# Kernel optimization log

Hardware: AMD Instinct MI355X
Metric: run time of the kernel (lower is better)

The kernel has to match this reference:

```python
import jax, jax.numpy as jnp
import numpy as np

EMB_DIM = 256
N_PTS = 2048  # decoder output points
LN_EPS = 1e-5


def setup_inputs() -> dict:
    key = jax.random.key(0)
    ks = jax.random.split(key, 20)
    B, N = 16, 4096

    def w(k, shape, fan_in):
        return (jax.random.normal(k, shape, dtype=jnp.float32) / np.sqrt(fan_in)).astype(jnp.float32)

    return {
        "in_pc": jax.random.normal(ks[0], (B, N, 3), dtype=jnp.float32),
        # encoder: 1x1 convs == per-point linear over channels
        "conv1_w": w(ks[1], (64, 3), 3),     "conv1_b": jnp.zeros((64,), jnp.float32),
        "conv2_w": w(ks[2], (128, 64), 64),  "conv2_b": jnp.zeros((128,), jnp.float32),
        "conv3_w": w(ks[3], (1024, 256), 256), "conv3_b": jnp.zeros((1024,), jnp.float32),
        "fc_enc_w": w(ks[4], (EMB_DIM, 1024), 1024), "fc_enc_b": jnp.zeros((EMB_DIM,), jnp.float32),
        # decoder
        "fc1_w": w(ks[5], (512, EMB_DIM), EMB_DIM), "fc1_b": jnp.zeros((512,), jnp.float32),
        "fc2_w": w(ks[6], (1024, 512), 512),        "fc2_b": jnp.zeros((1024,), jnp.float32),
        "fc3_w": w(ks[7], (3 * N_PTS, 1024), 1024), "fc3_b": jnp.zeros((3 * N_PTS,), jnp.float32),
        "ln_g": jnp.ones((3 * N_PTS,), jnp.float32), "ln_b": jnp.zeros((3 * N_PTS,), jnp.float32),
    }


def _pointwise(x, w, b):
    # x: (B, Cin, N), w: (Cout, Cin) -> (B, Cout, N)   (Conv1d with kernel=1)
    return jnp.einsum('bcn,oc->bon', x, w) + b[None, :, None]


def _chamfer(p, q):
    # p: (B,N,3), q: (B,M,3). Squared-L2 pairwise distance + min reductions.
    p2 = jnp.sum(p * p, axis=-1)                      # (B,N)
    q2 = jnp.sum(q * q, axis=-1)                      # (B,M)
    d = p2[:, :, None] + q2[:, None, :] - 2.0 * jnp.einsum('bnd,bmd->bnm', p, q)  # (B,N,M)
    return jnp.min(d, axis=2), jnp.min(d, axis=1)     # (B,N), (B,M)


def reference(in_pc, conv1_w, conv1_b, conv2_w, conv2_b, conv3_w, conv3_b,
              fc_enc_w, fc_enc_b, fc1_w, fc1_b, fc2_w, fc2_b, fc3_w, fc3_b,
              ln_g, ln_b):
    B, N, _ = in_pc.shape
    # ---- encoder ----
    xyz = jnp.transpose(in_pc, (0, 2, 1))            # (B,3,N)
    x = jax.nn.relu(_pointwise(xyz, conv1_w, conv1_b))   # (B,64,N)
    x = jax.nn.relu(_pointwise(x, conv2_w, conv2_b))     # (B,128,N)
    gfeat = jnp.max(x, axis=2, keepdims=True)            # (B,128,1) adaptive_max_pool1d(x,1)
    x0 = jnp.concatenate([x, jnp.broadcast_to(gfeat, (B, 128, N))], axis=1)  # (B,256,N)
    x = jax.nn.relu(_pointwise(x0, conv3_w, conv3_b))    # (B,1024,N)
    x = jnp.max(x, axis=2)                               # (B,1024)
    emb = x @ fc_enc_w.T + fc_enc_b                      # (B,EMB_DIM)
    # ---- decoder ----
    h = jax.nn.relu(emb @ fc1_w.T + fc1_b)               # (B,512)
    h = jax.nn.relu(h @ fc2_w.T + fc2_b)                 # (B,1024)
    h = h @ fc3_w.T + fc3_b                              # (B,3*N_PTS)
    mu = jnp.mean(h, axis=-1, keepdims=True)
    var = jnp.mean((h - mu) ** 2, axis=-1, keepdims=True)
    h = (h - mu) * jax.lax.rsqrt(var + LN_EPS) * ln_g + ln_b
    out_pc = h.reshape(B, -1, 3)                         # (B,N_PTS,3)
    # ---- chamfer reconstruction loss ----
    d1, d2 = _chamfer(in_pc, out_pc)
    loss = jnp.mean(d1) + jnp.mean(d2)
    return (x0, emb, out_pc, loss)
```

## Files before the change

### kernel.cpp

```cpp
#include <hip/hip_runtime.h>

#define OUT_X0   0
#define OUT_EMB  16777216
#define OUT_OPC  16781312
#define OUT_LOSS 16879616

#define OFF_GFEAT 0
#define OFF_POOL  8192
#define OFF_GCON  73728
#define OFF_EMB   139264
#define OFF_HD1   155648
#define OFF_HD2   188416
#define OFF_H3    253952
#define OFF_OPC   647168
#define OFF_D1M   1040384
#define OFF_D2M   1302528
#define OFF_PS    1433600
#define OFF_W3BF  1433984
#define OFF_CNT   1958272
#define H2_BYTES  (16u*1024*1024)

typedef short short8 __attribute__((ext_vector_type(8)));
typedef float f32x4  __attribute__((ext_vector_type(4)));

__device__ __forceinline__ unsigned short f2bf(float f){
  unsigned u = __float_as_uint(f);
  return (unsigned short)((u + 0x7FFFu + ((u >> 16) & 1u)) >> 16);
}

__global__ __launch_bounds__(256) void conv12_mfma(
    const float* __restrict__ in_pc,
    const float* __restrict__ w1, const float* __restrict__ b1,
    const float* __restrict__ w2, const float* __restrict__ b2,
    float* __restrict__ x0, unsigned short* __restrict__ h2b,
    unsigned* __restrict__ gfeatU,
    const float* __restrict__ w3, unsigned* __restrict__ w3bf)
{
  __shared__ unsigned short w2s[8192];
  __shared__ unsigned short h1s[8192];
  __shared__ float b2s[128];
  __shared__ unsigned gmax[128];
  int tid = threadIdx.x, bid = blockIdx.x;
  if (bid >= 512){
    int i = (bid-512)*256 + tid;
    float2 v = ((const float2*)w3)[i];
    w3bf[i] = (unsigned)f2bf(v.x) | ((unsigned)f2bf(v.y)<<16);
    return;
  }
  int b = bid >> 5;
  int nt0 = (bid & 31)*128;
  for (int i = tid; i < 2048; i += 256){
    int ch = i >> 4, q = i & 15;
    float4 v = ((const float4*)w2)[i];
    unsigned lo = (unsigned)f2bf(v.x) | ((unsigned)f2bf(v.y)<<16);
    unsigned hi = (unsigned)f2bf(v.z) | ((unsigned)f2bf(v.w)<<16);
    int byte = (ch*128 + q*8) ^ ((ch&7)<<4);
    *(uint2*)((char*)w2s + byte) = make_uint2(lo, hi);
  }
  if (tid < 128){ b2s[tid] = b2[tid]; gmax[tid] = 0u; }
  {
    int pt = tid & 127;
    int qb = (tid >> 7) * 16;
    int idx = b*4096 + nt0 + pt;
    const float* p = in_pc + (size_t)idx*3;
    float px=p[0], py=p[1], pz=p[2];
    unsigned hp[16];
    #pragma unroll
    for (int q=0;q<16;q++){
      int c = (qb + q)*2;
      float v0 = fmaxf(fmaf(w1[c*3  ],px, fmaf(w1[c*3+1],py, fmaf(w1[c*3+2],pz, b1[c  ]))), 0.f);
      float v1 = fmaxf(fmaf(w1[c*3+3],px, fmaf(w1[c*3+4],py, fmaf(w1[c*3+5],pz, b1[c+1]))), 0.f);
      hp[q] = (unsigned)f2bf(v0) | ((unsigned)f2bf(v1)<<16);
    }
    #pragma unroll
    for (int t=0;t<4;t++){
      int byte = (pt*128 + qb*4 + t*16) ^ ((pt&7)<<4);
      *(uint4*)((char*)h1s + byte) = make_uint4(hp[t*4],hp[t*4+1],hp[t*4+2],hp[t*4+3]);
    }
  }
  __syncthreads();
  int lane = tid & 63, w = tid >> 6;
  int g = lane >> 4, p15 = lane & 15;
  f32x4 acc[8][2] = {};
  #pragma unroll
  for (int ks=0; ks<2; ks++){
    int kb = (ks*32 + g*8)*2;
    short8 bfr[2];
    #pragma unroll
    for (int nf=0;nf<2;nf++){
      int pt = w*32 + nf*16 + p15;
      bfr[nf] = *(const short8*)((const char*)h1s + ((pt*128 + kb) ^ ((pt&7)<<4)));
    }
    #pragma unroll
    for (int mf=0;mf<8;mf++){
      int ch = mf*16 + p15;
      short8 af = *(const short8*)((const char*)w2s + ((ch*128 + kb) ^ ((ch&7)<<4)));
      acc[mf][0] = __builtin_amdgcn_mfma_f32_16x16x32_bf16(af, bfr[0], acc[mf][0], 0,0,0);
      acc[mf][1] = __builtin_amdgcn_mfma_f32_16x16x32_bf16(af, bfr[1], acc[mf][1], 0,0,0);
    }
  }
  int n_base = nt0 + w*32;
  #pragma unroll
  for (int mf=0; mf<8; mf++){
    int ch0 = mf*16 + g*4;
    float bias[4];
    #pragma unroll
    for (int j=0;j<4;j++) bias[j] = b2s[ch0+j];
    float vm[4] = {0.f,0.f,0.f,0.f};
    #pragma unroll
    for (int nf=0; nf<2; nf++){
      int n = n_base + nf*16 + p15;
      float v[4];
      #pragma unroll
      for (int j=0;j<4;j++){
        v[j] = fmaxf(acc[mf][nf][j] + bias[j], 0.f);
        vm[j] = fmaxf(vm[j], v[j]);
        x0[((size_t)(b*256 + ch0 + j))*4096 + n] = v[j];
      }
      unsigned lo = (unsigned)f2bf(v[0]) | ((unsigned)f2bf(v[1])<<16);
      unsigned hi = (unsigned)f2bf(v[2]) | ((unsigned)f2bf(v[3])<<16);
      *(uint2*)&h2b[((size_t)(b*4096 + n))*128 + ch0] = make_uint2(lo, hi);
    }
    #pragma unroll
    for (int j=0;j<4;j++){
      float m = vm[j];
      m = fmaxf(m, __shfl_xor(m,1));
      m = fmaxf(m, __shfl_xor(m,2));
      m = fmaxf(m, __shfl_xor(m,4));
      m = fmaxf(m, __shfl_xor(m,8));
      if (p15==0) atomicMax(&gmax[ch0+j], __float_as_uint(m));
    }
  }
  __syncthreads();
  if (tid < 128) atomicMax(&gfeatU[b*128 + tid], gmax[tid]);
}

__global__ __launch_bounds__(256) void bcast_gcon(
    const unsigned* __restrict__ gfeatU, float* __restrict__ x0,
    const float* __restrict__ w3, const float* __restrict__ b3,
    float* __restrict__ gcon)
{
  __shared__ float gf[2048];
  int tid = threadIdx.x;
  if (blockIdx.x < 8192){
    unsigned U = blockIdx.x*256 + tid;
    int n4 = U & 1023, c = (U >> 10) & 127, b = U >> 17;
    float g = __uint_as_float(gfeatU[b*128+c]);
    float4 v = {g,g,g,g};
    ((float4*)x0)[(((size_t)b*256 + 128 + c)*4096)/4 + n4] = v;
  } else {
    for (int i=tid;i<2048;i+=256) gf[i] = __uint_as_float(gfeatU[i]);
    __syncthreads();
    int o = (blockIdx.x - 8192)*256 + tid;
    float bias = b3[o];
    float acc[16];
    #pragma unroll
    for (int b=0;b<16;b++) acc[b]=bias;
    for (int c=0;c<128;c++){
      float wv = w3[(size_t)o*256 + 128 + c];
      #pragma unroll
      for (int b=0;b<16;b++) acc[b] += gf[b*128+c]*wv;
    }
    #pragma unroll
    for (int b=0;b<16;b++) gcon[b*1024+o] = acc[b];
  }
}

__global__ __launch_bounds__(512) void conv3_pool(
    const unsigned short* __restrict__ h2b, const unsigned short* __restrict__ w3b,
    const float* __restrict__ gcon, unsigned* __restrict__ pooled)
{
  __shared__ unsigned short Al[128*128];
  __shared__ unsigned short Bl[128*128];
  int mt = blockIdx.x, b = blockIdx.y;
  int tid = threadIdx.x;
  {
    const uint4* src = (const uint4*)(h2b + ((size_t)b*4096 + mt*128)*128);
    #pragma unroll
    for (int i=0;i<4;i++){
      int idx = i*512 + tid;
      int r = idx>>4, kc = idx&15;
      uint4 v = src[idx];
      int byte = (r*256 + kc*16) ^ ((r&7)<<4);
      *(uint4*)((char*)Al + byte) = v;
    }
  }
  int lane = tid & 63, wid = tid >> 6;
  int wm = wid >> 2, wn = wid & 3;
  int mbase = wm*64, nbase = wn*32;
  for (int nt=0; nt<8; nt++){
    if (nt) __syncthreads();
    {
      #pragma unroll
      for (int i=0;i<4;i++){
        int idx = i*512 + tid;
        int c = idx>>4, kc = idx&15;
        uint4 v = *(const uint4*)(w3b + ((size_t)(nt*128+c)*256 + kc*8));
        int byte = (c*256 + kc*16) ^ ((c&7)<<4);
        *(uint4*)((char*)Bl + byte) = v;
      }
    }
    __syncthreads();
    f32x4 acc[4][2] = {};
    #pragma unroll
    for (int ks=0;ks<4;ks++){
      int kb = (ks*32 + (lane>>4)*8)*2;
      short8 af[4], bfr[2];
      #pragma unroll
      for (int mi=0;mi<4;mi++){
        int row = mbase + mi*16 + (lane&15);
        af[mi] = *(const short8*)((const char*)Al + ((row*256 + kb) ^ ((row&7)<<4)));
      }
      #pragma unroll
      for (int ni=0;ni<2;ni++){
        int col = nbase + ni*16 + (lane&15);
        bfr[ni] = *(const short8*)((const char*)Bl + ((col*256 + kb) ^ ((col&7)<<4)));
      }
      #pragma unroll
      for (int mi=0;mi<4;mi++){
        #pragma unroll
        for (int ni=0;ni<2;ni++)
          acc[mi][ni] = __builtin_amdgcn_mfma_f32_16x16x32_bf16(af[mi], bfr[ni], acc[mi][ni], 0,0,0);
      }
    }
    #pragma unroll
    for (int ni=0;ni<2;ni++){
      int o = nt*128 + nbase + ni*16 + (lane&15);
      float g = gcon[b*1024 + o];
      float m = 0.f;
      #pragma unroll
      for (int mi=0;mi<4;mi++){
        f32x4 a = acc[mi][ni];
        #pragma unroll
        for (int r=0;r<4;r++){ float v = a[r]+g; m = fmaxf(m, v); }
      }
      m = fmaxf(m, 0.f);
      m = fmaxf(m, __shfl_xor(m, 16));
      m = fmaxf(m, __shfl_xor(m, 32));
      if (lane < 16) atomicMax(&pooled[(size_t)b*1024+o], __float_as_uint(m));
    }
  }
}

__global__ __launch_bounds__(256) void conv12_f32(
    const float* __restrict__ in_pc,
    const float* __restrict__ w1, const float* __restrict__ b1,
    const float* __restrict__ w2, const float* __restrict__ b2,
    float* __restrict__ x0, unsigned* __restrict__ gfeatU)
{
  __shared__ unsigned gmax[32];
  int tid = threadIdx.x;
  if (tid < 32) gmax[tid] = 0u;
  __syncthreads();
  int idx = blockIdx.x*256 + tid;
  int b = idx >> 12, n = idx & 4095;
  int gy = blockIdx.y;
  int lane = tid & 63;
  const float* p = in_pc + (size_t)idx*3;
  float px=p[0], py=p[1], pz=p[2];
  float h1[64];
  #pragma unroll
  for (int c=0;c<64;c++)
    h1[c] = fmaxf(w1[c*3]*px + w1[c*3+1]*py + w1[c*3+2]*pz + b1[c], 0.f);
  #pragma unroll
  for (int j=0;j<32;j++){
    int o = gy*32 + j;
    float a = b2[o];
    #pragma unroll
    for (int c=0;c<64;c++) a += w2[o*64+c]*h1[c];
    a = fmaxf(a, 0.f);
    x0[((size_t)b*256 + o)*4096 + n] = a;
    float m = a;
    #pragma unroll
    for (int off=32; off; off>>=1) m = fmaxf(m, __shfl_xor(m, off));
    if (lane==0) atomicMax(&gmax[j], __float_as_uint(m));
  }
  __syncthreads();
  if (tid < 32) atomicMax(&gfeatU[b*128 + gy*32 + tid], gmax[tid]);
}

__global__ __launch_bounds__(256) void conv3n(
    const float* __restrict__ x0, const unsigned* __restrict__ gfeatU,
    const float* __restrict__ w3, const float* __restrict__ b3,
    unsigned* __restrict__ pooled)
{
  __shared__ float wrow[8][256];
  int b = blockIdx.x >> 7, og = (blockIdx.x & 127)*8, tid = threadIdx.x;
  for (int i=tid;i<2048;i+=256){ int j=i>>8, c=i&255; wrow[j][c]=w3[(size_t)(og+j)*256+c]; }
  __syncthreads();
  float gconst[8];
  #pragma unroll
  for (int j=0;j<8;j++){
    float g = b3[og+j];
    for (int c=0;c<128;c++) g += __uint_as_float(gfeatU[b*128+c])*wrow[j][128+c];
    gconst[j] = g;
  }
  const float* xb = x0 + (size_t)b*256*4096;
  float m[8];
  #pragma unroll
  for (int j=0;j<8;j++) m[j]=0.f;
  for (int n=tid;n<4096;n+=256){
    float v[8];
    #pragma unroll
    for (int j=0;j<8;j++) v[j]=gconst[j];
    for (int c=0;c<128;c++){
      float xv = xb[(size_t)c*4096 + n];
      #pragma unroll
      for (int j=0;j<8;j++) v[j] += xv*wrow[j][c];
    }
    #pragma unroll
    for (int j=0;j<8;j++) m[j] = fmaxf(m[j], v[j]);
  }
  #pragma unroll
  for (int j=0;j<8;j++){
    float v = m[j];
    for (int off=32; off; off>>=1) v = fmaxf(v, __shfl_xor(v, off));
    if ((tid&63)==0) atomicMax(&pooled[(size_t)b*1024+og+j], __float_as_uint(v));
  }
}

template<bool RELU>
__global__ __launch_bounds__(256) void fc_wave16(
    const float* __restrict__ A, const float* __restrict__ W,
    const float* __restrict__ bias, float* __restrict__ out,
    float* __restrict__ out2, int K, int O)
{
  int lane = threadIdx.x & 63, w = threadIdx.x >> 6;
  int o = blockIdx.x*4 + w;
  const float* Wr = W + (size_t)o*K;
  float acc[16];
  #pragma unroll
  for (int b=0;b<16;b++) acc[b]=0.f;
  for (int k = lane*4; k < K; k += 256){
    float4 wv = *(const float4*)&Wr[k];
    #pragma unroll
    for (int b=0;b<16;b++){
      float4 av = *(const float4*)&A[(size_t)b*K + k];
      acc[b] += wv.x*av.x + wv.y*av.y + wv.z*av.z + wv.w*av.w;
    }
  }
  #pragma unroll
  for (int b=0;b<16;b++){
    float v = acc[b];
    #pragma unroll
    for (int off=32; off; off>>=1) v += __shfl_xor(v, off);
    if (lane==0){
      v += bias[o];
      if (RELU) v = fmaxf(v, 0.f);
      out[(size_t)b*O+o] = v;
      if (out2) out2[(size_t)b*O+o] = v;
    }
  }
}

__global__ __launch_bounds__(256) void lnorm(
    const float* __restrict__ h3, const float* __restrict__ g,
    const float* __restrict__ be, float* __restrict__ outf,
    float* __restrict__ outb, int* __restrict__ cnt)
{
  int b = blockIdx.x, tid = threadIdx.x;
  if (b==0 && tid==0) *cnt = 0;
  const float* x = h3 + b*6144;
  float s=0.f, s2=0.f;
  for (int i=tid;i<6144;i+=256){ float v=x[i]; s+=v; s2+=v*v; }
  for (int off=32; off; off>>=1){ s += __shfl_xor(s,off); s2 += __shfl_xor(s2,off); }
  __shared__ float red[8];
  int lane = tid&63, wid = tid>>6;
  if (lane==0){ red[wid]=s; red[4+wid]=s2; }
  __syncthreads();
  s  = red[0]+red[1]+red[2]+red[3];
  s2 = red[4]+red[5]+red[6]+red[7];
  float mu  = s * (1.f/6144.f);
  float var = s2 * (1.f/6144.f) - mu*mu;
  float inv = rsqrtf(var + 1e-5f);
  for (int i=tid;i<6144;i+=256){
    float v = (x[i]-mu)*inv*g[i] + be[i];
    outf[b*6144+i] = v;
    outb[b*6144+i] = v;
  }
}

__global__ __launch_bounds__(256) void chamfer_all(
    const float* __restrict__ in_pc, const float* __restrict__ opc,
    unsigned* __restrict__ d1m, unsigned* __restrict__ d2m)
{
  __shared__ float sX[256], sY[256], sZ[256], sQ[256];
  int bid = blockIdx.x, tid = threadIdx.x;
  const float* stage;
  const float* qry;
  unsigned* outp;
  if (bid < 2048){
    int xt = bid & 15, b = (bid >> 4) & 15, mt = bid >> 8;
    stage = opc + b*6144 + mt*768;
    qry   = in_pc + ((size_t)b*4096 + xt*256 + tid)*3;
    outp  = d1m + b*4096 + xt*256 + tid;
  } else {
    int r = bid - 2048;
    int xt = r & 7, b = (r >> 3) & 15, nt = r >> 7;
    stage = in_pc + ((size_t)b*4096 + nt*256)*3;
    qry   = opc + b*6144 + (xt*256 + tid)*3;
    outp  = d2m + b*2048 + xt*256 + tid;
  }
  {
    const float* S = stage + tid*3;
    float x=S[0], y=S[1], z=S[2];
    sX[tid]=-2.f*x; sY[tid]=-2.f*y; sZ[tid]=-2.f*z; sQ[tid]=x*x+y*y+z*z;
  }
  __syncthreads();
  float qx=qry[0], qy=qry[1], qz=qry[2];
  float p2 = qx*qx + qy*qy + qz*qz;
  float ma=3.0e38f, mb=3.0e38f, mc=3.0e38f, md=3.0e38f;
  #pragma unroll 4
  for (int i=0;i<64;i++){
    float4 X = *(const float4*)&sX[i*4];
    float4 Y = *(const float4*)&sY[i*4];
    float4 Z = *(const float4*)&sZ[i*4];
    float4 Q = *(const float4*)&sQ[i*4];
    float t;
    t = fmaf(qx,X.x, fmaf(qy,Y.x, fmaf(qz,Z.x, Q.x))); ma = fminf(ma,t);
    t = fmaf(qx,X.y, fmaf(qy,Y.y, fmaf(qz,Z.y, Q.y))); mb = fminf(mb,t);
    t = fmaf(qx,X.z, fmaf(qy,Y.z, fmaf(qz,Z.z, Q.z))); mc = fminf(mc,t);
    t = fmaf(qx,X.w, fmaf(qy,Y.w, fmaf(qz,Z.w, Q.w))); md = fminf(md,t);
  }
  float d = fmaxf(p2 + fminf(fminf(ma,mb), fminf(mc,md)), 0.f);
  atomicMin(outp, __float_as_uint(d));
}

__global__ __launch_bounds__(256) void sum_loss(
    const unsigned* __restrict__ d1m, const unsigned* __restrict__ d2m,
    float* __restrict__ ps, int* __restrict__ cnt, float* __restrict__ out)
{
  int bid = blockIdx.x, tid = threadIdx.x;
  __shared__ float red[4];
  __shared__ int last;
  {
    const unsigned* src = (bid<64) ? (d1m + bid*1024) : (d2m + (size_t)(bid-64)*1024);
    float s = 0.f;
    for (int i=tid;i<1024;i+=256) s += __uint_as_float(src[i]);
    for (int off=32; off; off>>=1) s += __shfl_xor(s,off);
    if ((tid&63)==0) red[tid>>6]=s;
    __syncthreads();
    if (tid==0){
      ps[bid] = red[0]+red[1]+red[2]+red[3];
      __threadfence();
      last = (atomicAdd(cnt, 1) == 95);
    }
    __syncthreads();
  }
  if (!last) return;
  __threadfence();
  float v = 0.f;
  if (tid < 64) v = ps[tid] * (1.0f/65536.0f);
  else if (tid < 96) v = ps[tid] * (1.0f/32768.0f);
  for (int off=32; off; off>>=1) v += __shfl_xor(v,off);
  __syncthreads();
  if ((tid&63)==0) red[tid>>6]=v;
  __syncthreads();
  if (tid==0) out[0] = red[0]+red[1]+red[2]+red[3];
}

extern "C" void kernel_launch(void* const* d_in, const int* in_sizes, int n_in,
                              void* d_out, int out_size, void* d_ws, size_t ws_size,
                              hipStream_t stream)
{
  (void)in_sizes; (void)n_in; (void)out_size;
  const float* in_pc = (const float*)d_in[0];
  const float* w1   = (const float*)d_in[1];
  const float* b1   = (const float*)d_in[2];
  const float* w2   = (const float*)d_in[3];
  const float* b2   = (const float*)d_in[4];
  const float* w3   = (const float*)d_in[5];
  const float* b3   = (const float*)d_in[6];
  const float* wenc = (const float*)d_in[7];
  const float* benc = (const float*)d_in[8];
  const float* wf1  = (const float*)d_in[9];
  const float* bfc1 = (const float*)d_in[10];
  const float* wf2  = (const float*)d_in[11];
  const float* bfc2 = (const float*)d_in[12];
  const float* wf3  = (const float*)d_in[13];
  const float* bfc3 = (const float*)d_in[14];
  const float* lng  = (const float*)d_in[15];
  const float* lnb  = (const float*)d_in[16];
  float* out = (float*)d_out;

  bool big = ws_size >= (size_t)(H2_BYTES + 2*1024*1024);
  char* ws = (char*)d_ws;
  unsigned short* h2b = (unsigned short*)ws;
  char* small = ws + (big ? H2_BYTES : 0);

  unsigned* gfeatU = (unsigned*)(small + OFF_GFEAT);
  float* pooled = (float*)(small + OFF_POOL);
  float* gcon = (float*)(small + OFF_GCON);
  float* emb  = (float*)(small + OFF_EMB);
  float* hd1  = (float*)(small + OFF_HD1);
  float* hd2  = (float*)(small + OFF_HD2);
  float* h3   = (float*)(small + OFF_H3);
  float* opc  = (float*)(small + OFF_OPC);
  unsigned* d1m = (unsigned*)(small + OFF_D1M);
  unsigned* d2m = (unsigned*)(small + OFF_D2M);
  float* ps   = (float*)(small + OFF_PS);
  unsigned short* w3b = (unsigned short*)(small + OFF_W3BF);
  int* cnt = (int*)(small + OFF_CNT);

  hipMemsetAsync(small + OFF_GFEAT, 0, 8192 + 65536, stream);
  hipMemsetAsync(small + OFF_D1M, 0x7F, 262144 + 131072, stream);

  if (big){
    conv12_mfma<<<1024, 256, 0, stream>>>(in_pc, w1, b1, w2, b2, out, h2b, gfeatU,
                                          w3, (unsigned*)w3b);
    bcast_gcon<<<8196, 256, 0, stream>>>(gfeatU, out, w3, b3, gcon);
    conv3_pool<<<dim3(32,16), 512, 0, stream>>>(h2b, w3b, gcon, (unsigned*)pooled);
  } else {
    conv12_f32<<<dim3(256,4), 256, 0, stream>>>(in_pc, w1, b1, w2, b2, out, gfeatU);
    bcast_gcon<<<8196, 256, 0, stream>>>(gfeatU, out, w3, b3, gcon);
    conv3n<<<2048, 256, 0, stream>>>(out, gfeatU, w3, b3, (unsigned*)pooled);
  }
  fc_wave16<false><<<64,   256, 0, stream>>>(pooled, wenc, benc, emb, out + OUT_EMB, 1024, 256);
  fc_wave16<true ><<<128,  256, 0, stream>>>(emb, wf1, bfc1, hd1, nullptr, 256, 512);
  fc_wave16<true ><<<256,  256, 0, stream>>>(hd1, wf2, bfc2, hd2, nullptr, 512, 1024);
  fc_wave16<false><<<1536, 256, 0, stream>>>(hd2, wf3, bfc3, h3, nullptr, 1024, 6144);
  lnorm<<<16, 256, 0, stream>>>(h3, lng, lnb, opc, out + OUT_OPC, cnt);
  chamfer_all<<<4096, 256, 0, stream>>>(in_pc, opc, d1m, d2m);
  sum_loss<<<96, 256, 0, stream>>>(d1m, d2m, ps, cnt, out + OUT_LOSS);
}
```

Measured before the change: 166.1 us.

## Fold memsets into conv12, replace gfeat atomics with per-block maxima, packed FMA chamfer

The two hipMemsetAsync calls on the fast path are removed, and extra blocks in conv12_mfma now zero the pooled buffer, fill the chamfer min buffers and reset the counter. The global atomicMax on gfeat is replaced by per-block partial maxima written to a new bmax buffer, which bcast_gcon reduces over 32 entries per channel. The chamfer inner loop uses v_pk_fma_f32 inline asm to process two distances per instruction. The trade-offs are a larger workspace threshold, redundant bmax reads in every broadcast thread, and reliance on kernel ordering so that the initialisation finishes before later kernels run.

```diff
diff --git a/kernel.cpp b/kernel.cpp
--- a/kernel.cpp
+++ b/kernel.cpp
@@ -18,14 +18,22 @@
 #define OFF_PS    1433600
 #define OFF_W3BF  1433984
 #define OFF_CNT   1958272
+#define OFF_BMAX  1958400
 #define H2_BYTES  (16u*1024*1024)
 
 typedef short short8 __attribute__((ext_vector_type(8)));
 typedef float f32x4  __attribute__((ext_vector_type(4)));
+typedef float f32x2  __attribute__((ext_vector_type(2)));
 
 __device__ __forceinline__ unsigned short f2bf(float f){
   unsigned u = __float_as_uint(f);
   return (unsigned short)((u + 0x7FFFu + ((u >> 16) & 1u)) >> 16);
+}
+
+__device__ __forceinline__ f32x2 pkfma(f32x2 a, f32x2 b, f32x2 c){
+  f32x2 d;
+  asm("v_pk_fma_f32 %0, %1, %2, %3" : "=v"(d) : "v"(a), "v"(b), "v"(c));
+  return d;
 }
 
 __global__ __launch_bounds__(256) void conv12_mfma(
@@ -33,14 +41,25 @@
     const float* __restrict__ w1, const float* __restrict__ b1,
     const float* __restrict__ w2, const float* __restrict__ b2,
     float* __restrict__ x0, unsigned short* __restrict__ h2b,
-    unsigned* __restrict__ gfeatU,
-    const float* __restrict__ w3, unsigned* __restrict__ w3bf)
+    unsigned* __restrict__ bmax,
+    const float* __restrict__ w3, unsigned* __restrict__ w3bf,
+    char* __restrict__ small)
 {
   __shared__ unsigned short w2s[8192];
   __shared__ unsigned short h1s[8192];
   __shared__ float b2s[128];
   __shared__ unsigned gmax[128];
   int tid = threadIdx.x, bid = blockIdx.x;
+  if (bid >= 1024){
+    int i = (bid-1024)*256 + tid;
+    if (i < 4096) ((uint4*)(small + OFF_POOL))[i] = make_uint4(0u,0u,0u,0u);
+    int j = i - 4096;
+    if (j >= 0 && j < 24576)
+      ((uint4*)(small + OFF_D1M))[j] =
+        make_uint4(0x7F7F7F7Fu,0x7F7F7F7Fu,0x7F7F7F7Fu,0x7F7F7F7Fu);
+    if (i == 28672) *(int*)(small + OFF_CNT) = 0;
+    return;
+  }
   if (bid >= 512){
     int i = (bid-512)*256 + tid;
     float2 v = ((const float2*)w3)[i];
@@ -132,10 +151,164 @@
     }
   }
   __syncthreads();
-  if (tid < 128) atomicMax(&gfeatU[b*128 + tid], gmax[tid]);
+  if (tid < 128) bmax[(size_t)bid*128 + tid] = gmax[tid];
 }
 
 __global__ __launch_bounds__(256) void bcast_gcon(
+    const unsigned* __restrict__ bmax, float* __restrict__ x0,
+    const float* __restrict__ w3, const float* __restrict__ b3,
+    float* __restrict__ gcon)
+{
+  __shared__ float gf[2048];
+  int tid = threadIdx.x;
+  if (blockIdx.x < 8192){
+    unsigned U = blockIdx.x*256 + tid;
+    int n4 = U & 1023, c = (U >> 10) & 127, b = U >> 17;
+    float g = 0.f;
+    #pragma unroll 8
+    for (int t=0;t<32;t++)
+      g = fmaxf(g, __uint_as_float(bmax[((size_t)(b*32+t))*128 + c]));
+    float4 v = {g,g,g,g};
+    ((float4*)x0)[(((size_t)b*256 + 128 + c)*4096)/4 + n4] = v;
+  } else {
+    for (int i=tid;i<2048;i+=256){
+      int b = i>>7, c = i&127;
+      float g = 0.f;
+      #pragma unroll 8
+      for (int t=0;t<32;t++)
+        g = fmaxf(g, __uint_as_float(bmax[((size_t)(b*32+t))*128 + c]));
+      gf[i] = g;
+    }
+    __syncthreads();
+    int o = (blockIdx.x - 8192)*256 + tid;
+    float bias = b3[o];
+    float acc[16];
+    #pragma unroll
+    for (int b=0;b<16;b++) acc[b]=bias;
+    for (int c=0;c<128;c++){
+      float wv = w3[(size_t)o*256 + 128 + c];
+      #pragma unroll
+      for (int b=0;b<16;b++) acc[b] += gf[b*128+c]*wv;
+    }
+    #pragma unroll
+    for (int b=0;b<16;b++) gcon[b*1024+o] = acc[b];
+  }
+}
+
+__global__ __launch_bounds__(512) void conv3_pool(
+    const unsigned short* __restrict__ h2b, const unsigned short* __restrict__ w3b,
+    const float* __restrict__ gcon, unsigned* __restrict__ pooled)
+{
+  __shared__ unsigned short Al[128*128];
+  __shared__ unsigned short Bl[128*128];
+  int mt = blockIdx.x, b = blockIdx.y;
+  int tid = threadIdx.x;
+  {
+    const uint4* src = (const uint4*)(h2b + ((size_t)b*4096 + mt*128)*128);
+    #pragma unroll
+    for (int i=0;i<4;i++){
+      int idx = i*512 + tid;
+      int r = idx>>4, kc = idx&15;
+      uint4 v = src[idx];
+      int byte = (r*256 + kc*16) ^ ((r&7)<<4);
+      *(uint4*)((char*)Al + byte) = v;
+    }
+  }
+  int lane = tid & 63, wid = tid >> 6;
+  int wm = wid >> 2, wn = wid & 3;
+  int mbase = wm*64, nbase = wn*32;
+  for (int nt=0; nt<8; nt++){
+    if (nt) __syncthreads();
+    {
+      #pragma unroll
+      for (int i=0;i<4;i++){
+        int idx = i*512 + tid;
+        int c = idx>>4, kc = idx&15;
+        uint4 v = *(const uint4*)(w3b + ((size_t)(nt*128+c)*256 + kc*8));
+        int byte = (c*256 + kc*16) ^ ((c&7)<<4);
+        *(uint4*)((char*)Bl + byte) = v;
+      }
+    }
+    __syncthreads();
+    f32x4 acc[4][2] = {};
+    #pragma unroll
+    for (int ks=0;ks<4;ks++){
+      int kb = (ks*32 + (lane>>4)*8)*2;
+      short8 af[4], bfr[2];
+      #pragma unroll
+      for (int mi=0;mi<4;mi++){
+        int row = mbase + mi*16 + (lane&15);
+        af[mi] = *(const short8*)((const char*)Al + ((row*256 + kb) ^ ((row&7)<<4)));
+      }
+      #pragma unroll
+      for (int ni=0;ni<2;ni++){
+        int col = nbase + ni*16 + (lane&15);
+        bfr[ni] = *(const short8*)((const char*)Bl + ((col*256 + kb) ^ ((col&7)<<4)));
+      }
+      #pragma unroll
+      for (int mi=0;mi<4;mi++){
+        #pragma unroll
+        for (int ni=0;ni<2;ni++)
+          acc[mi][ni] = __builtin_amdgcn_mfma_f32_16x16x32_bf16(af[mi], bfr[ni], acc[mi][ni], 0,0,0);
+      }
+    }
+    #pragma unroll
+    for (int ni=0;ni<2;ni++){
+      int o = nt*128 + nbase + ni*16 + (lane&15);
+      float g = gcon[b*1024 + o];
+      float m = 0.f;
+      #pragma unroll
+      for (int mi=0;mi<4;mi++){
+        f32x4 a = acc[mi][ni];
+        #pragma unroll
+        for (int r=0;r<4;r++){ float v = a[r]+g; m = fmaxf(m, v); }
+      }
+      m = fmaxf(m, 0.f);
+      m = fmaxf(m, __shfl_xor(m, 16));
+      m = fmaxf(m, __shfl_xor(m, 32));
+      if (lane < 16) atomicMax(&pooled[(size_t)b*1024+o], __float_as_uint(m));
+    }
+  }
+}
+
+__global__ __launch_bounds__(256) void conv12_f32(
+    const float* __restrict__ in_pc,
+    const float* __restrict__ w1, const float* __restrict__ b1,
+    const float* __restrict__ w2, const float* __restrict__ b2,
+    float* __restrict__ x0, unsigned* __restrict__ gfeatU)
+{
+  __shared__ unsigned gmax[32];
+  int tid = threadIdx.x;
+  if (tid < 32) gmax[tid] = 0u;
+  __syncthreads();
+  int idx = blockIdx.x*256 + tid;
+  int b = idx >> 12, n = idx & 4095;
+  int gy = blockIdx.y;
+  int lane = tid & 63;
+  const float* p = in_pc + (size_t)idx*3;
+  float px=p[0], py=p[1], pz=p[2];
+  float h1[64];
+  #pragma unroll
+  for (int c=0;c<64;c++)
+    h1[c] = fmaxf(w1[c*3]*px + w1[c*3+1]*py + w1[c*3+2]*pz + b1[c], 0.f);
+  #pragma unroll
+  for (int j=0;j<32;j++){
+    int o = gy*32 + j;
+    float a = b2[o];
+    #pragma unroll
+    for (int c=0;c<64;c++) a += w2[o*64+c]*h1[c];
+    a = fmaxf(a, 0.f);
+    x0[((size_t)b*256 + o)*4096 + n] = a;
+    float m = a;
+    #pragma unroll
+    for (int off=32; off; off>>=1) m = fmaxf(m, __shfl_xor(m, off));
+    if (lane==0) atomicMax(&gmax[j], __float_as_uint(m));
+  }
+  __syncthreads();
+  if (tid < 32) atomicMax(&gfeatU[b*128 + gy*32 + tid], gmax[tid]);
+}
+
+__global__ __launch_bounds__(256) void bcast_gcon_fb(
     const unsigned* __restrict__ gfeatU, float* __restrict__ x0,
     const float* __restrict__ w3, const float* __restrict__ b3,
     float* __restrict__ gcon)
@@ -164,119 +337,6 @@
     #pragma unroll
     for (int b=0;b<16;b++) gcon[b*1024+o] = acc[b];
   }
-}
-
-__global__ __launch_bounds__(512) void conv3_pool(
-    const unsigned short* __restrict__ h2b, const unsigned short* __restrict__ w3b,
-    const float* __restrict__ gcon, unsigned* __restrict__ pooled)
-{
-  __shared__ unsigned short Al[128*128];
-  __shared__ unsigned short Bl[128*128];
-  int mt = blockIdx.x, b = blockIdx.y;
-  int tid = threadIdx.x;
-  {
-    const uint4* src = (const uint4*)(h2b + ((size_t)b*4096 + mt*128)*128);
-    #pragma unroll
-    for (int i=0;i<4;i++){
-      int idx = i*512 + tid;
-      int r = idx>>4, kc = idx&15;
-      uint4 v = src[idx];
-      int byte = (r*256 + kc*16) ^ ((r&7)<<4);
-      *(uint4*)((char*)Al + byte) = v;
-    }
-  }
-  int lane = tid & 63, wid = tid >> 6;
-  int wm = wid >> 2, wn = wid & 3;
-  int mbase = wm*64, nbase = wn*32;
-  for (int nt=0; nt<8; nt++){
-    if (nt) __syncthreads();
-    {
-      #pragma unroll
-      for (int i=0;i<4;i++){
-        int idx = i*512 + tid;
-        int c = idx>>4, kc = idx&15;
-        uint4 v = *(const uint4*)(w3b + ((size_t)(nt*128+c)*256 + kc*8));
-        int byte = (c*256 + kc*16) ^ ((c&7)<<4);
-        *(uint4*)((char*)Bl + byte) = v;
-      }
-    }
-    __syncthreads();
-    f32x4 acc[4][2] = {};
-    #pragma unroll
-    for (int ks=0;ks<4;ks++){
-      int kb = (ks*32 + (lane>>4)*8)*2;
-      short8 af[4], bfr[2];
-      #pragma unroll
-      for (int mi=0;mi<4;mi++){
-        int row = mbase + mi*16 + (lane&15);
-        af[mi] = *(const short8*)((const char*)Al + ((row*256 + kb) ^ ((row&7)<<4)));
-      }
-      #pragma unroll
-      for (int ni=0;ni<2;ni++){
-        int col = nbase + ni*16 + (lane&15);
-        bfr[ni] = *(const short8*)((const char*)Bl + ((col*256 + kb) ^ ((col&7)<<4)));
-      }
-      #pragma unroll
-      for (int mi=0;mi<4;mi++){
-        #pragma unroll
-        for (int ni=0;ni<2;ni++)
-          acc[mi][ni] = __builtin_amdgcn_mfma_f32_16x16x32_bf16(af[mi], bfr[ni], acc[mi][ni], 0,0,0);
-      }
-    }
-    #pragma unroll
-    for (int ni=0;ni<2;ni++){
-      int o = nt*128 + nbase + ni*16 + (lane&15);
-      float g = gcon[b*1024 + o];
-      float m = 0.f;
-      #pragma unroll
-      for (int mi=0;mi<4;mi++){
-        f32x4 a = acc[mi][ni];
-        #pragma unroll
-        for (int r=0;r<4;r++){ float v = a[r]+g; m = fmaxf(m, v); }
-      }
-      m = fmaxf(m, 0.f);
-      m = fmaxf(m, __shfl_xor(m, 16));
-      m = fmaxf(m, __shfl_xor(m, 32));
-      if (lane < 16) atomicMax(&pooled[(size_t)b*1024+o], __float_as_uint(m));
-    }
-  }
-}
-
-__global__ __launch_bounds__(256) void conv12_f32(
-    const float* __restrict__ in_pc,
-    const float* __restrict__ w1, const float* __restrict__ b1,
-    const float* __restrict__ w2, const float* __restrict__ b2,
-    float* __restrict__ x0, unsigned* __restrict__ gfeatU)
-{
-  __shared__ unsigned gmax[32];
-  int tid = threadIdx.x;
-  if (tid < 32) gmax[tid] = 0u;
-  __syncthreads();
-  int idx = blockIdx.x*256 + tid;
-  int b = idx >> 12, n = idx & 4095;
-  int gy = blockIdx.y;
-  int lane = tid & 63;
-  const float* p = in_pc + (size_t)idx*3;
-  float px=p[0], py=p[1], pz=p[2];
-  float h1[64];
-  #pragma unroll
-  for (int c=0;c<64;c++)
-    h1[c] = fmaxf(w1[c*3]*px + w1[c*3+1]*py + w1[c*3+2]*pz + b1[c], 0.f);
-  #pragma unroll
-  for (int j=0;j<32;j++){
-    int o = gy*32 + j;
-    float a = b2[o];
-    #pragma unroll
-    for (int c=0;c<64;c++) a += w2[o*64+c]*h1[c];
-    a = fmaxf(a, 0.f);
-    x0[((size_t)b*256 + o)*4096 + n] = a;
-    float m = a;
-    #pragma unroll
-    for (int off=32; off; off>>=1) m = fmaxf(m, __shfl_xor(m, off));
-    if (lane==0) atomicMax(&gmax[j], __float_as_uint(m));
-  }
-  __syncthreads();
-  if (tid < 32) atomicMax(&gfeatU[b*128 + gy*32 + tid], gmax[tid]);
 }
 
 __global__ __launch_bounds__(256) void conv3n(
@@ -409,18 +469,24 @@
   __syncthreads();
   float qx=qry[0], qy=qry[1], qz=qry[2];
   float p2 = qx*qx + qy*qy + qz*qz;
+  f32x2 qxv = {qx,qx}, qyv = {qy,qy}, qzv = {qz,qz};
   float ma=3.0e38f, mb=3.0e38f, mc=3.0e38f, md=3.0e38f;
   #pragma unroll 4
   for (int i=0;i<64;i++){
-    float4 X = *(const float4*)&sX[i*4];
-    float4 Y = *(const float4*)&sY[i*4];
-    float4 Z = *(const float4*)&sZ[i*4];
-    float4 Q = *(const float4*)&sQ[i*4];
-    float t;
-    t = fmaf(qx,X.x, fmaf(qy,Y.x, fmaf(qz,Z.x, Q.x))); ma = fminf(ma,t);
-    t = fmaf(qx,X.y, fmaf(qy,Y.y, fmaf(qz,Z.y, Q.y))); mb = fminf(mb,t);
-    t = fmaf(qx,X.z, fmaf(qy,Y.z, fmaf(qz,Z.z, Q.z))); mc = fminf(mc,t);
-    t = fmaf(qx,X.w, fmaf(qy,Y.w, fmaf(qz,Z.w, Q.w))); md = fminf(md,t);
+    f32x4 X = *(const f32x4*)&sX[i*4];
+    f32x4 Y = *(const f32x4*)&sY[i*4];
+    f32x4 Z = *(const f32x4*)&sZ[i*4];
+    f32x4 Q = *(const f32x4*)&sQ[i*4];
+    f32x2 t0 = __builtin_shufflevector(Q,Q,0,1);
+    f32x2 t1 = __builtin_shufflevector(Q,Q,2,3);
+    t0 = pkfma(qzv, __builtin_shufflevector(Z,Z,0,1), t0);
+    t1 = pkfma(qzv, __builtin_shufflevector(Z,Z,2,3), t1);
+    t0 = pkfma(qyv, __builtin_shufflevector(Y,Y,0,1), t0);
+    t1 = pkfma(qyv, __builtin_shufflevector(Y,Y,2,3), t1);
+    t0 = pkfma(qxv, __builtin_shufflevector(X,X,0,1), t0);
+    t1 = pkfma(qxv, __builtin_shufflevector(X,X,2,3), t1);
+    ma = fminf(ma, t0.x); mb = fminf(mb, t0.y);
+    mc = fminf(mc, t1.x); md = fminf(md, t1.y);
   }
   float d = fmaxf(p2 + fminf(fminf(ma,mb), fminf(mc,md)), 0.f);
   atomicMin(outp, __float_as_uint(d));
@@ -483,7 +549,7 @@
   const float* lnb  = (const float*)d_in[16];
   float* out = (float*)d_out;
 
-  bool big = ws_size >= (size_t)(H2_BYTES + 2*1024*1024);
+  bool big = ws_size >= (size_t)(H2_BYTES + 3*1024*1024);
   char* ws = (char*)d_ws;
   unsigned short* h2b = (unsigned short*)ws;
   char* small = ws + (big ? H2_BYTES : 0);
@@ -501,18 +567,19 @@
   float* ps   = (float*)(small + OFF_PS);
   unsigned short* w3b = (unsigned short*)(small + OFF_W3BF);
   int* cnt = (int*)(small + OFF_CNT);
-
-  hipMemsetAsync(small + OFF_GFEAT, 0, 8192 + 65536, stream);
-  hipMemsetAsync(small + OFF_D1M, 0x7F, 262144 + 131072, stream);
+  unsigned* bmax = (unsigned*)(small + OFF_BMAX);
 
   if (big){
-    conv12_mfma<<<1024, 256, 0, stream>>>(in_pc, w1, b1, w2, b2, out, h2b, gfeatU,
-                                          w3, (unsigned*)w3b);
-    bcast_gcon<<<8196, 256, 0, stream>>>(gfeatU, out, w3, b3, gcon);
+    conv12_mfma<<<1139, 256, 0, stream>>>(in_pc, w1, b1, w2, b2, out, h2b, bmax,
+                                          w3, (unsigned*)w3b, small);
+    bcast_gcon<<<8196, 256, 0, stream>>>(bmax, out, w3, b3, gcon);
     conv3_pool<<<dim3(32,16), 512, 0, stream>>>(h2b, w3b, gcon, (unsigned*)pooled);
   } else {
+    hipMemsetAsync(small + OFF_GFEAT, 0, 8192 + 65536, stream);
+    hipMemsetAsync(small + OFF_D1M, 0x7F, 262144 + 131072, stream);
+    hipMemsetAsync(small + OFF_CNT, 0, 4, stream);
     conv12_f32<<<dim3(256,4), 256, 0, stream>>>(in_pc, w1, b1, w2, b2, out, gfeatU);
-    bcast_gcon<<<8196, 256, 0, stream>>>(gfeatU, out, w3, b3, gcon);
+    bcast_gcon_fb<<<8196, 256, 0, stream>>>(gfeatU, out, w3, b3, gcon);
     conv3n<<<2048, 256, 0, stream>>>(out, gfeatU, w3, b3, (unsigned*)pooled);
   }
   fc_wave16<false><<<64,   256, 0, stream>>>(pooled, wenc, benc, emb, out + OUT_EMB, 1024, 256);
```

After: 231.2 us. 39.2% more time.
